# Optimization experiments

Hardware: AMD Instinct MI355X
Metric: run time of the kernel (lower is better)

The kernel has to match this reference:

```python
import jax, jax.numpy as jnp
import numpy as np

VOCAB = 28996
B, W, D, H = 16, 64, 256, 512


def setup_inputs() -> dict:
    key = jax.random.key(0)
    ks = jax.random.split(key, 8)
    s_ih = 1.0 / np.sqrt(H)
    return {
        "x": jax.random.normal(ks[0], (B, W, D), dtype=jnp.float32),
        "last_encoder_hidden_state": jax.random.normal(ks[1], (1, H), dtype=jnp.float32),
        "w_ih": jax.random.uniform(ks[2], (3 * H, D), jnp.float32, -s_ih, s_ih),
        "w_hh": jax.random.uniform(ks[3], (3 * H, H), jnp.float32, -s_ih, s_ih),
        "b_ih": jax.random.uniform(ks[4], (3 * H,), jnp.float32, -s_ih, s_ih),
        "b_hh": jax.random.uniform(ks[5], (3 * H,), jnp.float32, -s_ih, s_ih),
        "w_pred": jax.random.uniform(ks[6], (VOCAB, H), jnp.float32, -s_ih, s_ih),
        "b_pred": jax.random.uniform(ks[7], (VOCAB,), jnp.float32, -s_ih, s_ih),
    }


def reference(x, last_encoder_hidden_state, w_ih, w_hh, b_ih, b_hh, w_pred, b_pred):
    b, w, d = x.shape
    # The torch code carries a single [1,H] hidden state sequentially over ALL
    # batch rows and words (state flows across batch boundaries). Flatten to T steps.
    xf = x.reshape(b * w, d)
    xg = xf @ w_ih.T + b_ih  # [T, 3H] input gate pre-activations, batched GEMM

    def step(h, xg_t):
        gh = h @ w_hh.T + b_hh            # [3H]
        xr, xz, xn = jnp.split(xg_t, 3)
        hr, hz, hn = jnp.split(gh, 3)
        r = jax.nn.sigmoid(xr + hr)
        z = jax.nn.sigmoid(xz + hz)
        n = jnp.tanh(xn + r * hn)
        h_new = (1.0 - z) * n + z * h
        return h_new, h_new

    h0 = last_encoder_hidden_state[0]     # [H]
    _, hs = jax.lax.scan(step, h0, xg)    # hs: [T, H]
    preds = hs @ w_pred.T + b_pred        # [T, VOCAB]
    return preds.reshape(b, w, VOCAB)
```

## Files before the change

### kernel.cpp

```cpp
#include <hip/hip_runtime.h>
#include <hip/hip_bf16.h>
#include <cstdint>

#define VOCAB 28996
#define T_STEPS 1024
#define D_IN 256
#define HDIM 512

using f32x4 = __attribute__((ext_vector_type(4))) float;
using s16x8 = __attribute__((ext_vector_type(8))) short;

static __device__ __forceinline__ unsigned short f2bf(float f){
    unsigned u = __float_as_uint(f);
    u = u + 0x7FFFu + ((u >> 16) & 1u);
    return (unsigned short)(u >> 16);
}

#define SENT_U 0x7FC00001u

__global__ void init_hs_kernel(const float* __restrict__ h0, float* __restrict__ hs,
                               unsigned* __restrict__ ctrl){
    const int col = threadIdx.x;
    const int row = blockIdx.x;
    float v = (row == 0) ? h0[col] : __uint_as_float(SENT_U);
    hs[(size_t)row * HDIM + col] = v;
    if (row == 0 && col < 8) ctrl[col] = 0u;
}

__global__ void xg_kernel(const float* __restrict__ x, const float* __restrict__ w_ih,
                          const float* __restrict__ b_ih, float* __restrict__ xg){
    __shared__ float xs[8][D_IN];
    const int tid = threadIdx.x;
    const int i   = blockIdx.x * 256 + tid;
    const int t0  = blockIdx.y * 8;
    #pragma unroll
    for (int r = 0; r < 8; ++r)
        xs[r][tid] = x[(size_t)(t0 + r) * D_IN + tid];
    __syncthreads();

    float acc[8] = {0.f,0.f,0.f,0.f,0.f,0.f,0.f,0.f};
    const float* wrow = w_ih + (size_t)i * D_IN;
    for (int d = 0; d < D_IN; d += 4){
        float4 w4 = *(const float4*)(wrow + d);
        #pragma unroll
        for (int r = 0; r < 8; ++r){
            acc[r] += w4.x * xs[r][d]   + w4.y * xs[r][d+1]
                    + w4.z * xs[r][d+2] + w4.w * xs[r][d+3];
        }
    }
    const float b = b_ih[i];
    #pragma unroll
    for (int r = 0; r < 8; ++r)
        xg[(size_t)(t0 + r) * (3*HDIM) + i] = acc[r] + b;
}

#define LDW(G, P, s) \
    float G##s##0 = (P)[128*s + 0], G##s##1 = (P)[128*s + 1], \
          G##s##2 = (P)[128*s + 2], G##s##3 = (P)[128*s + 3];
#define PINW(G, s) \
    asm volatile("" : "+v"(G##s##0), "+v"(G##s##1), "+v"(G##s##2), "+v"(G##s##3));

#define GS(s, hh) { \
    ar += R##s##0*hh.x + R##s##1*hh.y + R##s##2*hh.z + R##s##3*hh.w; \
    az += Z##s##0*hh.x + Z##s##1*hh.y + Z##s##2*hh.z + Z##s##3*hh.w; \
    an += N##s##0*hh.x + N##s##1*hh.y + N##s##2*hh.z + N##s##3*hh.w; }

__launch_bounds__(512)
__attribute__((amdgpu_waves_per_eu(2, 2)))
__global__ void scan_kernel(const float* __restrict__ xg, const float* __restrict__ w_hh,
                            const float* __restrict__ b_hh, float* hs, unsigned* ctrl){
    __shared__ unsigned sh_rank;

    const int tid = threadIdx.x;
    if (tid == 0){
        unsigned xcc;
        asm volatile("s_getreg_b32 %0, hwreg(HW_REG_XCC_ID)" : "=s"(xcc));
        sh_rank = __hip_atomic_fetch_add(&ctrl[xcc & 7u], 1u, __ATOMIC_RELAXED,
                                         __HIP_MEMORY_SCOPE_AGENT);
    }
    __syncthreads();
    const unsigned rank = sh_rank;
    if (rank >= 32u) return;

    const int c  = tid & 31;
    const int jl = tid >> 5;
    const int j  = (int)rank * 16 + jl;

    const float* wrp = w_hh + (size_t)j * HDIM + 4*c;
    const float* wzp = w_hh + (size_t)(HDIM   + j) * HDIM + 4*c;
    const float* wnp = w_hh + (size_t)(2*HDIM + j) * HDIM + 4*c;
    LDW(R, wrp, 0) LDW(R, wrp, 1) LDW(R, wrp, 2) LDW(R, wrp, 3)
    LDW(Z, wzp, 0) LDW(Z, wzp, 1) LDW(Z, wzp, 2) LDW(Z, wzp, 3)
    LDW(N, wnp, 0) LDW(N, wnp, 1) LDW(N, wnp, 2) LDW(N, wnp, 3)
    PINW(R,0) PINW(R,1) PINW(R,2) PINW(R,3)
    PINW(Z,0) PINW(Z,1) PINW(Z,2) PINW(Z,3)
    PINW(N,0) PINW(N,1) PINW(N,2) PINW(N,3)

    float bhr = b_hh[j], bhz = b_hh[HDIM + j], bhn = b_hh[2*HDIM + j];
    asm volatile("" : "+v"(bhr), "+v"(bhz), "+v"(bhn));

    float xr_c = 0.f, xz_c = 0.f, xn_c = 0.f;
    if (c == 0){ xr_c = xg[j]; xz_c = xg[HDIM + j]; xn_c = xg[2*HDIM + j]; }

    const float* lanep = hs + 4*c;
    const float* jp    = hs + j;

    #pragma unroll 1
    for (int t = 0; t < T_STEPS; ++t){
        f32x4 h0, h1, h2, h3;
        float hj;
        int spins = 0;
        for (;;){
            asm volatile(
                "global_load_dwordx4 %0, %5, off nt\n\t"
                "global_load_dwordx4 %1, %5, off offset:512 nt\n\t"
                "global_load_dwordx4 %2, %5, off offset:1024 nt\n\t"
                "global_load_dwordx4 %3, %5, off offset:1536 nt\n\t"
                "global_load_dword   %4, %6, off nt\n\t"
                "s_waitcnt vmcnt(0)"
                : "=&v"(h0), "=&v"(h1), "=&v"(h2), "=&v"(h3), "=&v"(hj)
                : "v"(lanep), "v"(jp) : "memory");
            int ok = (__float_as_uint(h0.x) != SENT_U) & (__float_as_uint(h0.y) != SENT_U)
                   & (__float_as_uint(h0.z) != SENT_U) & (__float_as_uint(h0.w) != SENT_U)
                   & (__float_as_uint(h1.x) != SENT_U) & (__float_as_uint(h1.y) != SENT_U)
                   & (__float_as_uint(h1.z) != SENT_U) & (__float_as_uint(h1.w) != SENT_U)
                   & (__float_as_uint(h2.x) != SENT_U) & (__float_as_uint(h2.y) != SENT_U)
                   & (__float_as_uint(h2.z) != SENT_U) & (__float_as_uint(h2.w) != SENT_U)
                   & (__float_as_uint(h3.x) != SENT_U) & (__float_as_uint(h3.y) != SENT_U)
                   & (__float_as_uint(h3.z) != SENT_U) & (__float_as_uint(h3.w) != SENT_U)
                   & (__float_as_uint(hj)   != SENT_U);
            if (__all(ok)) break;
            if (++spins > 4000) return;
        }

        float ar = 0.f, az = 0.f, an = 0.f;
        GS(0, h0) GS(1, h1) GS(2, h2) GS(3, h3)
        #pragma unroll
        for (int m = 1; m < 32; m <<= 1){
            ar += __shfl_xor(ar, m);
            az += __shfl_xor(az, m);
            an += __shfl_xor(an, m);
        }

        if (c == 0){
            const float r  = 1.0f / (1.0f + __expf(-(xr_c + ar + bhr)));
            const float z  = 1.0f / (1.0f + __expf(-(xz_c + az + bhz)));
            const float nn = xn_c + r * (an + bhn);
            const float e  = __expf(2.0f * nn);
            const float th = 1.0f - 2.0f / (e + 1.0f);
            const float hnew = (1.0f - z) * th + z * hj;
            hs[(size_t)(t + 1) * HDIM + j] = hnew;
        }

        float xr_n = 0.f, xz_n = 0.f, xn_n = 0.f;
        if (c == 0 && t + 1 < T_STEPS){
            const float* xgn = xg + (size_t)(t + 1) * (3*HDIM);
            xr_n = xgn[j]; xz_n = xgn[HDIM + j]; xn_n = xgn[2*HDIM + j];
        }
        xr_c = xr_n; xz_c = xz_n; xn_c = xn_n;

        lanep += HDIM;
        jp    += HDIM;
    }
}

__launch_bounds__(256)
__global__ void pred_gemm_kernel(const float* __restrict__ hs, const float* __restrict__ w_pred,
                                 const float* __restrict__ b_pred, float* __restrict__ out){
    __shared__ unsigned short As[128 * 32];
    __shared__ unsigned short Bs[128 * 32];
    const int tid   = threadIdx.x;
    const int mtile = blockIdx.x;
    const int ntile = blockIdx.y;
    const int row  = tid >> 1, half = tid & 1;
    const int wave = tid >> 6, lane = tid & 63;
    const int wm = wave >> 1, wn = wave & 1;
    const int lr = lane & 15, kq = lane >> 4;

    f32x4 acc[4][4] = {};

    const float* Abase = hs + HDIM  + (size_t)(mtile * 128 + row) * HDIM;
    const int    nrow  = ntile * 128 + row;
    const float* Bbase = w_pred + (size_t)nrow * HDIM;

    for (int k0 = 0; k0 < HDIM; k0 += 32){
        {
            const float* srcp = Abase + k0 + half * 16;
            unsigned short* dst = &As[row * 32 + half * 16];
            #pragma unroll
            for (int q = 0; q < 4; ++q){
                float4 v = *(const float4*)(srcp + 4 * q);
                uint2 p;
                p.x = (unsigned)f2bf(v.x) | ((unsigned)f2bf(v.y) << 16);
                p.y = (unsigned)f2bf(v.z) | ((unsigned)f2bf(v.w) << 16);
                *(uint2*)(dst + 4 * q) = p;
            }
        }
        {
            unsigned short* dst = &Bs[row * 32 + half * 16];
            if (nrow < VOCAB){
                const float* srcp = Bbase + k0 + half * 16;
                #pragma unroll
                for (int q = 0; q < 4; ++q){
                    float4 v = *(const float4*)(srcp + 4 * q);
                    uint2 p;
                    p.x = (unsigned)f2bf(v.x) | ((unsigned)f2bf(v.y) << 16);
                    p.y = (unsigned)f2bf(v.z) | ((unsigned)f2bf(v.w) << 16);
                    *(uint2*)(dst + 4 * q) = p;
                }
            } else {
                uint2 zz; zz.x = 0u; zz.y = 0u;
                #pragma unroll
                for (int q = 0; q < 4; ++q) *(uint2*)(dst + 4 * q) = zz;
            }
        }
        __syncthreads();

        const unsigned short* Ab = &As[(wm * 64 + lr) * 32 + kq * 8];
        const unsigned short* Bb = &Bs[(wn * 64 + lr) * 32 + kq * 8];
        s16x8 af[4], bf[4];
        #pragma unroll
        for (int mf = 0; mf < 4; ++mf) af[mf] = *(const s16x8*)(Ab + mf * 16 * 32);
        #pragma unroll
        for (int nf = 0; nf < 4; ++nf) bf[nf] = *(const s16x8*)(Bb + nf * 16 * 32);
        #pragma unroll
        for (int mf = 0; mf < 4; ++mf){
            #pragma unroll
            for (int nf = 0; nf < 4; ++nf){
                acc[mf][nf] = __builtin_amdgcn_mfma_f32_16x16x32_bf16(af[mf], bf[nf], acc[mf][nf], 0, 0, 0);
            }
        }
        __syncthreads();
    }

    #pragma unroll
    for (int nf = 0; nf < 4; ++nf){
        const int n = ntile * 128 + wn * 64 + nf * 16 + lr;
        if (n >= VOCAB) continue;
        const float bp = b_pred[n];
        #pragma unroll
        for (int mf = 0; mf < 4; ++mf){
            const int m = mtile * 128 + wm * 64 + mf * 16 + kq * 4;
            #pragma unroll
            for (int q = 0; q < 4; ++q){
                out[(size_t)(m + q) * VOCAB + n] = acc[mf][nf][q] + bp;
            }
        }
    }
}

extern "C" void kernel_launch(void* const* d_in, const int* in_sizes, int n_in,
                              void* d_out, int out_size, void* d_ws, size_t ws_size,
                              hipStream_t stream){
    const float* x      = (const float*)d_in[0];
    const float* h0     = (const float*)d_in[1];
    const float* w_ih   = (const float*)d_in[2];
    const float* w_hh   = (const float*)d_in[3];
    const float* b_ih   = (const float*)d_in[4];
    const float* b_hh   = (const float*)d_in[5];
    const float* w_pred = (const float*)d_in[6];
    const float* b_pred = (const float*)d_in[7];
    float* out = (float*)d_out;

    float*    xg   = (float*)d_ws;
    float*    hs   = xg + (size_t)T_STEPS * (3*HDIM);
    unsigned* ctrl = (unsigned*)(hs + (size_t)(T_STEPS+1) * HDIM);

    hipLaunchKernelGGL(init_hs_kernel, dim3(T_STEPS + 1), dim3(HDIM), 0, stream, h0, hs, ctrl);
    hipLaunchKernelGGL(xg_kernel,      dim3(6, 128),      dim3(256),  0, stream, x, w_ih, b_ih, xg);
    hipLaunchKernelGGL(scan_kernel,    dim3(256),         dim3(512),  0, stream, xg, w_hh, b_hh, hs, ctrl);
    hipLaunchKernelGGL(pred_gemm_kernel, dim3(8, 227),    dim3(256),  0, stream, hs, w_pred, b_pred, out);
}
```

Measured before the change: 1.789 ms.

## Give each XCC a private hidden-state buffer and first-finisher copy-out

Each XCC now runs its own redundant GRU scan into a private hidden-state history, so polling and stores stay within that XCC's L2 instead of crossing dies. An LDS pad limits each CU to one block, and rows a few steps ahead are pre-touched so their cache lines are resident before polling. The first XCC to finish copies its history to the shared buffer and sets a done flag that makes the other XCCs exit early. The cost is eight times the init work and workspace, plus redundant compute that depends on the done-flag and timeout logic being correct.

```diff
diff --git a/kernel.cpp b/kernel.cpp
--- a/kernel.cpp
+++ b/kernel.cpp
@@ -18,13 +18,14 @@
 
 #define SENT_U 0x7FC00001u
 
-__global__ void init_hs_kernel(const float* __restrict__ h0, float* __restrict__ hs,
+__global__ void init_hs_kernel(const float* __restrict__ h0, float* __restrict__ hs_priv,
                                unsigned* __restrict__ ctrl){
     const int col = threadIdx.x;
     const int row = blockIdx.x;
+    const int cpy = blockIdx.y;
     float v = (row == 0) ? h0[col] : __uint_as_float(SENT_U);
-    hs[(size_t)row * HDIM + col] = v;
-    if (row == 0 && col < 8) ctrl[col] = 0u;
+    hs_priv[((size_t)cpy * (T_STEPS + 1) + row) * HDIM + col] = v;
+    if (row == 0 && cpy == 0 && col < 288) ctrl[col] = 0u;
 }
 
 __global__ void xg_kernel(const float* __restrict__ x, const float* __restrict__ w_ih,
@@ -65,22 +66,65 @@
     az += Z##s##0*hh.x + Z##s##1*hh.y + Z##s##2*hh.z + Z##s##3*hh.w; \
     an += N##s##0*hh.x + N##s##1*hh.y + N##s##2*hh.z + N##s##3*hh.w; }
 
+#define PRETOUCH(ROWP) { \
+    const float* pa_ = (ROWP) + 4*c; \
+    const float* pb_ = (ROWP) + j; \
+    asm volatile( \
+        "global_load_dword %0, %5, off\n\t" \
+        "global_load_dword %1, %5, off offset:512\n\t" \
+        "global_load_dword %2, %5, off offset:1024\n\t" \
+        "global_load_dword %3, %5, off offset:1536\n\t" \
+        "global_load_dword %4, %6, off" \
+        : "=&v"(p0), "=&v"(p1), "=&v"(p2), "=&v"(p3), "=&v"(p4) \
+        : "v"(pa_), "v"(pb_) : "memory"); }
+
+#define NTPOLL(H0,H1,H2,H3,HJ,LP,JP) \
+    asm volatile( \
+        "global_load_dwordx4 %0, %5, off nt\n\t" \
+        "global_load_dwordx4 %1, %5, off offset:512 nt\n\t" \
+        "global_load_dwordx4 %2, %5, off offset:1024 nt\n\t" \
+        "global_load_dwordx4 %3, %5, off offset:1536 nt\n\t" \
+        "global_load_dword   %4, %6, off nt\n\t" \
+        "s_waitcnt vmcnt(0)" \
+        : "=&v"(H0), "=&v"(H1), "=&v"(H2), "=&v"(H3), "=&v"(HJ) \
+        : "v"(LP), "v"(JP), "v"(p0), "v"(p1), "v"(p2), "v"(p3), "v"(p4) \
+        : "memory")
+
+#define SENTOK(H0,H1,H2,H3,HJ) \
+      ((__float_as_uint(H0.x) != SENT_U) & (__float_as_uint(H0.y) != SENT_U) \
+     & (__float_as_uint(H0.z) != SENT_U) & (__float_as_uint(H0.w) != SENT_U) \
+     & (__float_as_uint(H1.x) != SENT_U) & (__float_as_uint(H1.y) != SENT_U) \
+     & (__float_as_uint(H1.z) != SENT_U) & (__float_as_uint(H1.w) != SENT_U) \
+     & (__float_as_uint(H2.x) != SENT_U) & (__float_as_uint(H2.y) != SENT_U) \
+     & (__float_as_uint(H2.z) != SENT_U) & (__float_as_uint(H2.w) != SENT_U) \
+     & (__float_as_uint(H3.x) != SENT_U) & (__float_as_uint(H3.y) != SENT_U) \
+     & (__float_as_uint(H3.z) != SENT_U) & (__float_as_uint(H3.w) != SENT_U) \
+     & (__float_as_uint(HJ)   != SENT_U))
+
 __launch_bounds__(512)
 __attribute__((amdgpu_waves_per_eu(2, 2)))
 __global__ void scan_kernel(const float* __restrict__ xg, const float* __restrict__ w_hh,
-                            const float* __restrict__ b_hh, float* hs, unsigned* ctrl){
-    __shared__ unsigned sh_rank;
+                            const float* __restrict__ b_hh, float* hs_sh,
+                            float* hs_priv, unsigned* ctrl){
+    __shared__ volatile float lds_pad[21000];
+    __shared__ unsigned sh_rank, sh_xcc;
 
     const int tid = threadIdx.x;
+    lds_pad[tid] = 0.f;
     if (tid == 0){
         unsigned xcc;
         asm volatile("s_getreg_b32 %0, hwreg(HW_REG_XCC_ID)" : "=s"(xcc));
-        sh_rank = __hip_atomic_fetch_add(&ctrl[xcc & 7u], 1u, __ATOMIC_RELAXED,
+        xcc &= 7u;
+        sh_xcc  = xcc;
+        sh_rank = __hip_atomic_fetch_add(&ctrl[xcc * 32], 1u, __ATOMIC_RELAXED,
                                          __HIP_MEMORY_SCOPE_AGENT);
     }
     __syncthreads();
     const unsigned rank = sh_rank;
     if (rank >= 32u) return;
+
+    float* hsx = hs_priv + (size_t)sh_xcc * (T_STEPS + 1) * HDIM;
+    const unsigned* donep = ctrl + 256;
 
     const int c  = tid & 31;
     const int jl = tid >> 5;
@@ -102,8 +146,20 @@
     float xr_c = 0.f, xz_c = 0.f, xn_c = 0.f;
     if (c == 0){ xr_c = xg[j]; xz_c = xg[HDIM + j]; xn_c = xg[2*HDIM + j]; }
 
-    const float* lanep = hs + 4*c;
-    const float* jp    = hs + j;
+    {
+        float s = 0.f;
+        #pragma unroll
+        for (int r = 0; r < 3; ++r){
+            const float* pp = hsx + (size_t)r * HDIM;
+            s += pp[4*c] + pp[4*c + 128] + pp[4*c + 256] + pp[4*c + 384] + pp[j];
+        }
+        asm volatile("" :: "v"(s));
+    }
+    float p0, p1, p2, p3, p4;
+    { const float* pp = hsx + (size_t)3 * HDIM; PRETOUCH(pp); }
+
+    const float* lanep = hsx + 4*c;
+    const float* jp    = hsx + j;
 
     #pragma unroll 1
     for (int t = 0; t < T_STEPS; ++t){
@@ -111,26 +167,27 @@
         float hj;
         int spins = 0;
         for (;;){
-            asm volatile(
-                "global_load_dwordx4 %0, %5, off nt\n\t"
-                "global_load_dwordx4 %1, %5, off offset:512 nt\n\t"
-                "global_load_dwordx4 %2, %5, off offset:1024 nt\n\t"
-                "global_load_dwordx4 %3, %5, off offset:1536 nt\n\t"
-                "global_load_dword   %4, %6, off nt\n\t"
-                "s_waitcnt vmcnt(0)"
-                : "=&v"(h0), "=&v"(h1), "=&v"(h2), "=&v"(h3), "=&v"(hj)
-                : "v"(lanep), "v"(jp) : "memory");
-            int ok = (__float_as_uint(h0.x) != SENT_U) & (__float_as_uint(h0.y) != SENT_U)
-                   & (__float_as_uint(h0.z) != SENT_U) & (__float_as_uint(h0.w) != SENT_U)
-                   & (__float_as_uint(h1.x) != SENT_U) & (__float_as_uint(h1.y) != SENT_U)
-                   & (__float_as_uint(h1.z) != SENT_U) & (__float_as_uint(h1.w) != SENT_U)
-                   & (__float_as_uint(h2.x) != SENT_U) & (__float_as_uint(h2.y) != SENT_U)
-                   & (__float_as_uint(h2.z) != SENT_U) & (__float_as_uint(h2.w) != SENT_U)
-                   & (__float_as_uint(h3.x) != SENT_U) & (__float_as_uint(h3.y) != SENT_U)
-                   & (__float_as_uint(h3.z) != SENT_U) & (__float_as_uint(h3.w) != SENT_U)
-                   & (__float_as_uint(hj)   != SENT_U);
+            NTPOLL(h0, h1, h2, h3, hj, lanep, jp);
+            int ok = SENTOK(h0, h1, h2, h3, hj);
             if (__all(ok)) break;
-            if (++spins > 4000) return;
+            if ((++spins & 255) == 0){
+                unsigned dn;
+                asm volatile("global_load_dword %0, %1, off nt\n\ts_waitcnt vmcnt(0)"
+                             : "=&v"(dn) : "v"(donep) : "memory");
+                if (__any(dn != 0)) return;
+                if (spins > 6000) return;
+            }
+        }
+
+        if (t + 4 <= T_STEPS){
+            const float* pp = hsx + (size_t)(t + 4) * HDIM;
+            PRETOUCH(pp);
+        }
+
+        float xr_n = 0.f, xz_n = 0.f, xn_n = 0.f;
+        if (c == 0 && t + 1 < T_STEPS){
+            const float* xgn = xg + (size_t)(t + 1) * (3*HDIM);
+            xr_n = xgn[j]; xz_n = xgn[HDIM + j]; xn_n = xgn[2*HDIM + j];
         }
 
         float ar = 0.f, az = 0.f, an = 0.f;
@@ -141,7 +198,6 @@
             az += __shfl_xor(az, m);
             an += __shfl_xor(an, m);
         }
-
         if (c == 0){
             const float r  = 1.0f / (1.0f + __expf(-(xr_c + ar + bhr)));
             const float z  = 1.0f / (1.0f + __expf(-(xz_c + az + bhz)));
@@ -149,19 +205,43 @@
             const float e  = __expf(2.0f * nn);
             const float th = 1.0f - 2.0f / (e + 1.0f);
             const float hnew = (1.0f - z) * th + z * hj;
-            hs[(size_t)(t + 1) * HDIM + j] = hnew;
-        }
-
-        float xr_n = 0.f, xz_n = 0.f, xn_n = 0.f;
-        if (c == 0 && t + 1 < T_STEPS){
-            const float* xgn = xg + (size_t)(t + 1) * (3*HDIM);
-            xr_n = xgn[j]; xz_n = xgn[HDIM + j]; xn_n = xgn[2*HDIM + j];
+            hsx[(size_t)(t + 1) * HDIM + j] = hnew;
         }
         xr_c = xr_n; xz_c = xz_n; xn_c = xn_n;
-
-        lanep += HDIM;
-        jp    += HDIM;
-    }
+        lanep += HDIM; jp += HDIM;
+    }
+
+    {
+        f32x4 a0, a1, a2, a3; float aj;
+        int spins = 0;
+        for (;;){
+            NTPOLL(a0, a1, a2, a3, aj, lanep, jp);
+            int ok = SENTOK(a0, a1, a2, a3, aj);
+            if (__all(ok)) break;
+            if (++spins > 6000) return;
+        }
+    }
+
+    {
+        const int p = (int)rank * 512 + tid;
+        #pragma unroll
+        for (int k = 0; k < 8; k += 2){
+            const size_t i0 = 128 + (size_t)p + (size_t)k * 16384;
+            const size_t i1 = i0 + 16384;
+            const float* s0 = (const float*)hsx + i0 * 4;
+            const float* s1 = (const float*)hsx + i1 * 4;
+            f32x4 v0, v1;
+            asm volatile("global_load_dwordx4 %0, %2, off nt\n\t"
+                         "global_load_dwordx4 %1, %3, off nt\n\t"
+                         "s_waitcnt vmcnt(0)"
+                         : "=&v"(v0), "=&v"(v1) : "v"(s0), "v"(s1) : "memory");
+            *(f32x4*)((float*)hs_sh + i0 * 4) = v0;
+            *(f32x4*)((float*)hs_sh + i1 * 4) = v1;
+        }
+    }
+    if (tid == 0)
+        __hip_atomic_store((unsigned*)donep, 1u, __ATOMIC_RELAXED,
+                           __HIP_MEMORY_SCOPE_AGENT);
 }
 
 __launch_bounds__(256)
@@ -262,12 +342,13 @@
     const float* b_pred = (const float*)d_in[7];
     float* out = (float*)d_out;
 
-    float*    xg   = (float*)d_ws;
-    float*    hs   = xg + (size_t)T_STEPS * (3*HDIM);
-    unsigned* ctrl = (unsigned*)(hs + (size_t)(T_STEPS+1) * HDIM);
-
-    hipLaunchKernelGGL(init_hs_kernel, dim3(T_STEPS + 1), dim3(HDIM), 0, stream, h0, hs, ctrl);
-    hipLaunchKernelGGL(xg_kernel,      dim3(6, 128),      dim3(256),  0, stream, x, w_ih, b_ih, xg);
-    hipLaunchKernelGGL(scan_kernel,    dim3(256),         dim3(512),  0, stream, xg, w_hh, b_hh, hs, ctrl);
-    hipLaunchKernelGGL(pred_gemm_kernel, dim3(8, 227),    dim3(256),  0, stream, hs, w_pred, b_pred, out);
-}
+    float*    xg      = (float*)d_ws;
+    float*    hs_sh   = xg + (size_t)T_STEPS * (3*HDIM);
+    float*    hs_priv = hs_sh + (size_t)(T_STEPS + 1) * HDIM;
+    unsigned* ctrl    = (unsigned*)(hs_priv + 8 * (size_t)(T_STEPS + 1) * HDIM);
+
+    hipLaunchKernelGGL(init_hs_kernel, dim3(T_STEPS + 1, 8), dim3(HDIM), 0, stream, h0, hs_priv, ctrl);
+    hipLaunchKernelGGL(xg_kernel,      dim3(6, 128),         dim3(256), 0, stream, x, w_ih, b_ih, xg);
+    hipLaunchKernelGGL(scan_kernel,    dim3(256),            dim3(512), 0, stream, xg, w_hh, b_hh, hs_sh, hs_priv, ctrl);
+    hipLaunchKernelGGL(pred_gemm_kernel, dim3(8, 227),       dim3(256), 0, stream, hs_sh, w_pred, b_pred, out);
+}
```

Measured after the change: 1.879 ms. +5.0%, slower.
